# Optimization experiments

Hardware: AMD Instinct MI355X
Metric: run time of the kernel (lower is better)

## Reference

```python
import jax, jax.numpy as jnp
import numpy as np

N_O = 50000
N_Q = 50000
E = 1_600_000
POS_DIM = 3
LATENT = 128
HEADS = 4
HEAD_DIM = 32
EDGE_IN = 3 * POS_DIM  # ['rel','q_pos','o_pos']


def setup_inputs() -> dict:
    key = jax.random.key(0)
    ks = jax.random.split(key, 12)
    h_obs = jax.random.normal(ks[0], (N_O, LATENT), dtype=jnp.float32)
    pos_obs = jax.random.uniform(ks[1], (N_O, POS_DIM), dtype=jnp.float32)
    pos_query = jax.random.uniform(ks[2], (N_Q, POS_DIM), dtype=jnp.float32)
    src = jax.random.randint(ks[3], (E,), 0, N_O, dtype=jnp.int32)
    dst = jnp.sort(jax.random.randint(ks[4], (E,), 0, N_Q, dtype=jnp.int32))
    s = 0.05
    W1 = jax.random.normal(ks[5], (EDGE_IN, LATENT), dtype=jnp.float32) * s
    b1 = jnp.zeros((LATENT,), dtype=jnp.float32)
    W2 = jax.random.normal(ks[6], (LATENT, HEADS), dtype=jnp.float32) * s
    b2 = jnp.zeros((HEADS,), dtype=jnp.float32)
    Wv = jax.random.normal(ks[7], (LATENT, HEADS * HEAD_DIM), dtype=jnp.float32) * s
    bv = jnp.zeros((HEADS * HEAD_DIM,), dtype=jnp.float32)
    log_sigma = jnp.float32(-2.0)
    return {"h_obs": h_obs, "pos_obs": pos_obs, "pos_query": pos_query,
            "src": src, "dst": dst,
            "W1": W1, "b1": b1, "W2": W2, "b2": b2,
            "Wv": Wv, "bv": bv, "log_sigma": log_sigma}


def _forward(h_obs, pos_obs, pos_query, src, dst, W1, b1, W2, b2, Wv, bv, log_sigma):
    pos_o = pos_obs[src]                      # [E, P]
    pos_q = pos_query[dst]                    # [E, P]
    rel = pos_q - pos_o
    edge_attr = jnp.concatenate([rel, pos_q, pos_o], axis=-1)   # [E, 3P]
    hid = jax.nn.relu(edge_attr @ W1 + b1)                      # [E, LATENT]
    logits = hid @ W2 + b2                                      # [E, H]
    dist2 = jnp.sum(rel * rel, axis=-1, keepdims=True)          # [E, 1]
    sigma = jnp.exp(log_sigma) + 1e-6
    logits = logits - dist2 / (2.0 * sigma * sigma)             # kernel log-weight
    # segment softmax over edges grouped by dst
    n_q = pos_query.shape[0]
    m = jax.ops.segment_max(logits, dst, num_segments=n_q)      # [N_q, H]
    ex = jnp.exp(logits - m[dst])
    denom = jax.ops.segment_sum(ex, dst, num_segments=n_q)      # [N_q, H]
    attn = ex / (denom[dst] + 1e-16)                            # [E, H]
    v = (h_obs @ Wv + bv).reshape(-1, HEADS, HEAD_DIM)          # [N_o, H, D]
    msg = attn[:, :, None] * v[src]                             # [E, H, D]
    out = jax.ops.segment_sum(msg, dst, num_segments=n_q)       # [N_q, H, D]
    return out.reshape(n_q, HEADS * HEAD_DIM)


def reference(h_obs, pos_obs, pos_query, src, dst, W1, b1, W2, b2, Wv, bv, log_sigma):
    return _forward(h_obs, pos_obs, pos_query, src, dst, W1, b1, W2, b2, Wv, bv, log_sigma)
```

## Files before the change

kernel.cpp:

```cpp
#include <hip/hip_runtime.h>
#include <hip/hip_bf16.h>
#include <cstdint>
#include <cstddef>

#define N_O 50000
#define N_Q 50000
#define NE  1600000

typedef __attribute__((ext_vector_type(8)))  short short8;
typedef __attribute__((ext_vector_type(16))) float f32x16;

__device__ inline unsigned short f2bf(float x) {
    __hip_bfloat16 hb = __float2bfloat16(x);
    return *reinterpret_cast<unsigned short*>(&hb);
}

__global__ void pack_kernel(const float* __restrict__ W1, const float* __restrict__ b1,
                            const float* __restrict__ W2, const float* __restrict__ b2,
                            const float* __restrict__ log_sigma,
                            unsigned short* __restrict__ W1cT,
                            unsigned short* __restrict__ W2tb,
                            float* __restrict__ scal) {
    int j = threadIdx.x;
    if (j < 128) {
        #pragma unroll
        for (int a = 0; a < 3; ++a) {
            W1cT[j * 8 + a]     = f2bf(W1[(3 + a) * 128 + j] + W1[a * 128 + j]);
            W1cT[j * 8 + 3 + a] = f2bf(W1[(6 + a) * 128 + j] - W1[a * 128 + j]);
        }
        W1cT[j * 8 + 6] = f2bf(b1[j]);
        W1cT[j * 8 + 7] = 0;
        #pragma unroll
        for (int hd = 0; hd < 4; ++hd)
            W2tb[hd * 128 + j] = f2bf(W2[j * 4 + hd]);
    } else if (j == 128) {
        float sigma = expf(log_sigma[0]) + 1e-6f;
        scal[0] = 1.0f / (2.0f * sigma * sigma);
        scal[1] = b2[0]; scal[2] = b2[1]; scal[3] = b2[2]; scal[4] = b2[3];
    }
}

__global__ void rowptr_kernel(const int* __restrict__ dst, int* __restrict__ rp) {
    int q = blockIdx.x * blockDim.x + threadIdx.x;
    if (q > N_Q) return;
    int lo = 0, hi = NE;
    while (lo < hi) {
        int mid = (lo + hi) >> 1;
        if (dst[mid] < q) lo = mid + 1; else hi = mid;
    }
    rp[q] = lo;
}

__global__ __launch_bounds__(256) void vproj_kernel(const float* __restrict__ h,
                                                    const float* __restrict__ Wv,
                                                    const float* __restrict__ bv,
                                                    unsigned short* __restrict__ v) {
    __shared__ float Ash[64 * 132];
    int t = threadIdx.x;
    int n0 = blockIdx.x * 64;
    #pragma unroll
    for (int rep = 0; rep < 8; ++rep) {
        int idx = rep * 256 + t;
        int row = idx >> 5, c4 = (idx & 31) * 4;
        float4 val = make_float4(0.f, 0.f, 0.f, 0.f);
        if (n0 + row < N_O) val = *(const float4*)(h + (size_t)(n0 + row) * 128 + c4);
        float* d = &Ash[row * 132 + c4];
        d[0] = val.x; d[1] = val.y; d[2] = val.z; d[3] = val.w;
    }
    __syncthreads();

    int cg = t & 15, rg = t >> 4;
    int c0 = cg * 8, r0 = rg * 4;
    float acc[4][8];
    #pragma unroll
    for (int i = 0; i < 4; ++i)
        #pragma unroll
        for (int j = 0; j < 8; ++j) acc[i][j] = 0.f;

    const float4* Wv4 = (const float4*)Wv;
    for (int k = 0; k < 128; ++k) {
        float4 b0 = Wv4[k * 32 + cg * 2];
        float4 b1v = Wv4[k * 32 + cg * 2 + 1];
        float bb[8] = {b0.x, b0.y, b0.z, b0.w, b1v.x, b1v.y, b1v.z, b1v.w};
        #pragma unroll
        for (int i = 0; i < 4; ++i) {
            float a = Ash[(r0 + i) * 132 + k];
            #pragma unroll
            for (int j = 0; j < 8; ++j) acc[i][j] += a * bb[j];
        }
    }

    float bvv[8];
    #pragma unroll
    for (int j = 0; j < 8; ++j) bvv[j] = bv[c0 + j];
    #pragma unroll
    for (int i = 0; i < 4; ++i) {
        int n = n0 + r0 + i;
        if (n < N_O) {
            uint4 o;
            __hip_bfloat162 t0 = __float22bfloat162_rn(
                make_float2(acc[i][0] + bvv[0], acc[i][1] + bvv[1]));
            __hip_bfloat162 t1 = __float22bfloat162_rn(
                make_float2(acc[i][2] + bvv[2], acc[i][3] + bvv[3]));
            __hip_bfloat162 t2 = __float22bfloat162_rn(
                make_float2(acc[i][4] + bvv[4], acc[i][5] + bvv[5]));
            __hip_bfloat162 t3 = __float22bfloat162_rn(
                make_float2(acc[i][6] + bvv[6], acc[i][7] + bvv[7]));
            o.x = *reinterpret_cast<unsigned int*>(&t0);
            o.y = *reinterpret_cast<unsigned int*>(&t1);
            o.z = *reinterpret_cast<unsigned int*>(&t2);
            o.w = *reinterpret_cast<unsigned int*>(&t3);
            *(uint4*)(v + (size_t)n * 128 + c0) = o;
        }
    }
}

__global__ __launch_bounds__(256) void edge_kernel(const float* __restrict__ pos_obs,
                                                   const float* __restrict__ pos_query,
                                                   const int* __restrict__ src,
                                                   const int* __restrict__ dst,
                                                   const unsigned short* __restrict__ W1cT,
                                                   const unsigned short* __restrict__ W2tb,
                                                   const float* __restrict__ scal,
                                                   float* __restrict__ logitsT) {
    __shared__ __align__(16) unsigned char smem[4 * 8448];
    int t = threadIdx.x;
    int wave = t >> 6, lane = t & 63;
    int i = lane & 31, h = lane >> 5;
    unsigned char* myrow = smem + wave * 8448 + i * 264;

    short8 zero8;
    #pragma unroll
    for (int k = 0; k < 8; ++k) zero8[k] = 0;

    short8 a1[4];
    #pragma unroll
    for (int b = 0; b < 4; ++b)
        a1[b] = (h == 0) ? *(const short8*)(W1cT + (32 * b + i) * 8) : zero8;

    short8 a2[8];
    #pragma unroll
    for (int m = 0; m < 8; ++m)
        a2[m] = (i < 4) ? *(const short8*)(W2tb + i * 128 + m * 16 + h * 8) : zero8;

    int e = blockIdx.x * 128 + wave * 32 + i;
    int s = src[e], d = dst[e];
    float pox = pos_obs[s * 3 + 0], poy = pos_obs[s * 3 + 1], poz = pos_obs[s * 3 + 2];
    float pqx = pos_query[d * 3 + 0], pqy = pos_query[d * 3 + 1], pqz = pos_query[d * 3 + 2];
    float rx = pqx - pox, ry = pqy - poy, rz = pqz - poz;
    float dist2 = rx * rx + ry * ry + rz * rz;

    short8 bea = zero8;
    if (h == 0) {
        bea[0] = (short)f2bf(pqx); bea[1] = (short)f2bf(pqy); bea[2] = (short)f2bf(pqz);
        bea[3] = (short)f2bf(pox); bea[4] = (short)f2bf(poy); bea[5] = (short)f2bf(poz);
        bea[6] = (short)0x3F80;
        bea[7] = 0;
    }

    f32x16 c1[4];
    #pragma unroll
    for (int b = 0; b < 4; ++b) {
        #pragma unroll
        for (int k = 0; k < 16; ++k) c1[b][k] = 0.0f;
        c1[b] = __builtin_amdgcn_mfma_f32_32x32x16_bf16(a1[b], bea, c1[b], 0, 0, 0);
    }

    #pragma unroll
    for (int b = 0; b < 4; ++b) {
        #pragma unroll
        for (int s_ = 0; s_ < 4; ++s_) {
            float x0 = fmaxf(c1[b][4 * s_ + 0], 0.f);
            float x1 = fmaxf(c1[b][4 * s_ + 1], 0.f);
            float x2 = fmaxf(c1[b][4 * s_ + 2], 0.f);
            float x3 = fmaxf(c1[b][4 * s_ + 3], 0.f);
            __hip_bfloat162 p0 = __float22bfloat162_rn(make_float2(x0, x1));
            __hip_bfloat162 p1 = __float22bfloat162_rn(make_float2(x2, x3));
            uint2 w;
            w.x = *reinterpret_cast<unsigned int*>(&p0);
            w.y = *reinterpret_cast<unsigned int*>(&p1);
            *(uint2*)(myrow + 64 * b + 16 * s_ + 8 * h) = w;
        }
    }

    f32x16 c2;
    #pragma unroll
    for (int k = 0; k < 16; ++k) c2[k] = 0.0f;
    #pragma unroll
    for (int m = 0; m < 8; ++m) {
        uint2 lo = *(const uint2*)(myrow + 32 * m + 16 * h);
        uint2 hi = *(const uint2*)(myrow + 32 * m + 16 * h + 8);
        union { unsigned int u[4]; short8 s; } bf;
        bf.u[0] = lo.x; bf.u[1] = lo.y; bf.u[2] = hi.x; bf.u[3] = hi.y;
        c2 = __builtin_amdgcn_mfma_f32_32x32x16_bf16(a2[m], bf.s, c2, 0, 0, 0);
    }

    if (h == 0) {
        float pen = dist2 * scal[0];
        logitsT[0 * NE + e] = c2[0] + scal[1] - pen;
        logitsT[1 * NE + e] = c2[1] + scal[2] - pen;
        logitsT[2 * NE + e] = c2[2] + scal[3] - pen;
        logitsT[3 * NE + e] = c2[3] + scal[4] - pen;
    }
}

__global__ __launch_bounds__(256) void attn_kernel(const __hip_bfloat162* __restrict__ vb,
                                                   const float* __restrict__ logitsT,
                                                   const int* __restrict__ src,
                                                   const int* __restrict__ rp,
                                                   float* __restrict__ out) {
    int t = threadIdx.x;
    int lane = t & 63;
    int q = blockIdx.x * 4 + (t >> 6);
    int s0 = rp[q], s1 = rp[q + 1];
    int h = lane >> 4, i = lane & 15;
    const float* lp = logitsT + (size_t)h * NE;

    float m = -INFINITY;
    for (int e = s0 + i; e < s1; e += 16) m = fmaxf(m, lp[e]);
    #pragma unroll
    for (int off = 8; off; off >>= 1) m = fmaxf(m, __shfl_xor(m, off));

    float sum = 0.f;
    for (int e = s0 + i; e < s1; e += 16) sum += __expf(lp[e] - m);
    #pragma unroll
    for (int off = 8; off; off >>= 1) sum += __shfl_xor(sum, off);
    float r = 1.0f / (sum + 1e-16f);

    float acc0 = 0.f, acc1 = 0.f;
    int e = s0;
    for (; e < s1 && (e & 3); ++e) {
        float w = __expf(lp[e] - m);
        float2 f = __bfloat1622float2(vb[(size_t)src[e] * 64 + lane]);
        acc0 += w * f.x; acc1 += w * f.y;
    }
    for (; e + 4 <= s1; e += 4) {
        float4 l4 = *(const float4*)(lp + e);
        int4 s4 = *(const int4*)(src + e);
        float w0 = __expf(l4.x - m);
        float w1 = __expf(l4.y - m);
        float w2 = __expf(l4.z - m);
        float w3 = __expf(l4.w - m);
        float2 f0 = __bfloat1622float2(vb[(size_t)s4.x * 64 + lane]);
        float2 f1 = __bfloat1622float2(vb[(size_t)s4.y * 64 + lane]);
        float2 f2 = __bfloat1622float2(vb[(size_t)s4.z * 64 + lane]);
        float2 f3 = __bfloat1622float2(vb[(size_t)s4.w * 64 + lane]);
        acc0 += w0 * f0.x + w1 * f1.x + w2 * f2.x + w3 * f3.x;
        acc1 += w0 * f0.y + w1 * f1.y + w2 * f2.y + w3 * f3.y;
    }
    for (; e < s1; ++e) {
        float w = __expf(lp[e] - m);
        float2 f = __bfloat1622float2(vb[(size_t)src[e] * 64 + lane]);
        acc0 += w * f.x; acc1 += w * f.y;
    }
    *(float2*)(out + (size_t)q * 128 + lane * 2) = make_float2(acc0 * r, acc1 * r);
}

extern "C" void kernel_launch(void* const* d_in, const int* in_sizes, int n_in,
                              void* d_out, int out_size, void* d_ws, size_t ws_size,
                              hipStream_t stream) {
    const float* h_obs     = (const float*)d_in[0];
    const float* pos_obs   = (const float*)d_in[1];
    const float* pos_query = (const float*)d_in[2];
    const int*   src       = (const int*)d_in[3];
    const int*   dst       = (const int*)d_in[4];
    const float* W1        = (const float*)d_in[5];
    const float* b1        = (const float*)d_in[6];
    const float* W2        = (const float*)d_in[7];
    const float* b2        = (const float*)d_in[8];
    const float* Wv        = (const float*)d_in[9];
    const float* bv        = (const float*)d_in[10];
    const float* log_sigma = (const float*)d_in[11];
    float* out = (float*)d_out;

    char* ws = (char*)d_ws;
    int*            rp      = (int*)(ws + 0);
    float*          scal    = (float*)(ws + 200192);
    unsigned short* W1cT    = (unsigned short*)(ws + 200256);
    unsigned short* W2tb    = (unsigned short*)(ws + 202304);
    unsigned short* vbuf    = (unsigned short*)(ws + 208640);
    float*          logitsT = (float*)(ws + 13008768);

    hipLaunchKernelGGL(pack_kernel, dim3(1), dim3(256), 0, stream,
                       W1, b1, W2, b2, log_sigma, W1cT, W2tb, scal);
    hipLaunchKernelGGL(rowptr_kernel, dim3((N_Q + 256) / 256), dim3(256), 0, stream,
                       dst, rp);
    hipLaunchKernelGGL(vproj_kernel, dim3((N_O + 63) / 64), dim3(256), 0, stream,
                       h_obs, Wv, bv, vbuf);
    hipLaunchKernelGGL(edge_kernel, dim3(NE / 128), dim3(256), 0, stream,
                       pos_obs, pos_query, src, dst, W1cT, W2tb, scal, logitsT);
    hipLaunchKernelGGL(attn_kernel, dim3(N_Q / 4), dim3(256), 0, stream,
                       (const __hip_bfloat162*)vbuf, logitsT, src, rp, out);
}
```

Before: 257.4 us.

## Merge edge, vproj and rowptr into one launch; cache softmax weights in LDS

Three independent kernels (edge MLP, value projection, row-pointer search) are folded into one launch that picks a body by block index. This removes two launch boundaries and lets the three jobs run concurrently on the GPU. In the attention kernel, segments with at most 256 edges now store their exp weights in shared memory during the sum pass, so the gather pass reads them back instead of re-reading the logits and recomputing exp. The fused kernel takes the larger shared-memory footprint for every block, and attention now uses extra LDS, which may lower occupancy.

```diff
diff --git a/kernel.cpp b/kernel.cpp
--- a/kernel.cpp
+++ b/kernel.cpp
@@ -6,6 +6,11 @@
 #define N_O 50000
 #define N_Q 50000
 #define NE  1600000
+
+#define EDGE_BLOCKS  (NE / 128)
+#define VP_BLOCKS    ((N_O + 63) / 64)
+#define RP_BLOCKS    ((N_Q + 256) / 256)
+#define WCAP 264
 
 typedef __attribute__((ext_vector_type(8)))  short short8;
 typedef __attribute__((ext_vector_type(16))) float f32x16;
@@ -40,8 +45,8 @@
     }
 }
 
-__global__ void rowptr_kernel(const int* __restrict__ dst, int* __restrict__ rp) {
-    int q = blockIdx.x * blockDim.x + threadIdx.x;
+__device__ void rowptr_body(int bid, const int* __restrict__ dst, int* __restrict__ rp) {
+    int q = bid * 256 + threadIdx.x;
     if (q > N_Q) return;
     int lo = 0, hi = NE;
     while (lo < hi) {
@@ -51,13 +56,13 @@
     rp[q] = lo;
 }
 
-__global__ __launch_bounds__(256) void vproj_kernel(const float* __restrict__ h,
-                                                    const float* __restrict__ Wv,
-                                                    const float* __restrict__ bv,
-                                                    unsigned short* __restrict__ v) {
-    __shared__ float Ash[64 * 132];
+__device__ void vproj_body(int bid, const float* __restrict__ h,
+                           const float* __restrict__ Wv,
+                           const float* __restrict__ bv,
+                           unsigned short* __restrict__ v,
+                           float* Ash ) {
     int t = threadIdx.x;
-    int n0 = blockIdx.x * 64;
+    int n0 = bid * 64;
     #pragma unroll
     for (int rep = 0; rep < 8; ++rep) {
         int idx = rep * 256 + t;
@@ -115,15 +120,15 @@
     }
 }
 
-__global__ __launch_bounds__(256) void edge_kernel(const float* __restrict__ pos_obs,
-                                                   const float* __restrict__ pos_query,
-                                                   const int* __restrict__ src,
-                                                   const int* __restrict__ dst,
-                                                   const unsigned short* __restrict__ W1cT,
-                                                   const unsigned short* __restrict__ W2tb,
-                                                   const float* __restrict__ scal,
-                                                   float* __restrict__ logitsT) {
-    __shared__ __align__(16) unsigned char smem[4 * 8448];
+__device__ void edge_body(int bid, const float* __restrict__ pos_obs,
+                          const float* __restrict__ pos_query,
+                          const int* __restrict__ src,
+                          const int* __restrict__ dst,
+                          const unsigned short* __restrict__ W1cT,
+                          const unsigned short* __restrict__ W2tb,
+                          const float* __restrict__ scal,
+                          float* __restrict__ logitsT,
+                          unsigned char* smem ) {
     int t = threadIdx.x;
     int wave = t >> 6, lane = t & 63;
     int i = lane & 31, h = lane >> 5;
@@ -143,7 +148,7 @@
     for (int m = 0; m < 8; ++m)
         a2[m] = (i < 4) ? *(const short8*)(W2tb + i * 128 + m * 16 + h * 8) : zero8;
 
-    int e = blockIdx.x * 128 + wave * 32 + i;
+    int e = bid * 128 + wave * 32 + i;
     int s = src[e], d = dst[e];
     float pox = pos_obs[s * 3 + 0], poy = pos_obs[s * 3 + 1], poz = pos_obs[s * 3 + 2];
     float pqx = pos_query[d * 3 + 0], pqy = pos_query[d * 3 + 1], pqz = pos_query[d * 3 + 2];
@@ -204,15 +209,41 @@
     }
 }
 
+__global__ __launch_bounds__(256) void fused_kernel(const float* __restrict__ pos_obs,
+                                                    const float* __restrict__ pos_query,
+                                                    const int* __restrict__ src,
+                                                    const int* __restrict__ dst,
+                                                    const unsigned short* __restrict__ W1cT,
+                                                    const unsigned short* __restrict__ W2tb,
+                                                    const float* __restrict__ scal,
+                                                    float* __restrict__ logitsT,
+                                                    const float* __restrict__ h_obs,
+                                                    const float* __restrict__ Wv,
+                                                    const float* __restrict__ bv,
+                                                    unsigned short* __restrict__ vbuf,
+                                                    int* __restrict__ rp) {
+    __shared__ __align__(16) unsigned char smem[33792];
+    int b = blockIdx.x;
+    if (b < EDGE_BLOCKS) {
+        edge_body(b, pos_obs, pos_query, src, dst, W1cT, W2tb, scal, logitsT, smem);
+    } else if (b < EDGE_BLOCKS + VP_BLOCKS) {
+        vproj_body(b - EDGE_BLOCKS, h_obs, Wv, bv, vbuf, (float*)smem);
+    } else {
+        rowptr_body(b - EDGE_BLOCKS - VP_BLOCKS, dst, rp);
+    }
+}
+
 __global__ __launch_bounds__(256) void attn_kernel(const __hip_bfloat162* __restrict__ vb,
                                                    const float* __restrict__ logitsT,
                                                    const int* __restrict__ src,
                                                    const int* __restrict__ rp,
                                                    float* __restrict__ out) {
+    __shared__ __align__(16) float wsh[4 * 4 * WCAP];
     int t = threadIdx.x;
-    int lane = t & 63;
-    int q = blockIdx.x * 4 + (t >> 6);
+    int lane = t & 63, wave = t >> 6;
+    int q = blockIdx.x * 4 + wave;
     int s0 = rp[q], s1 = rp[q + 1];
+    int cnt = s1 - s0;
     int h = lane >> 4, i = lane & 15;
     const float* lp = logitsT + (size_t)h * NE;
 
@@ -221,37 +252,75 @@
     #pragma unroll
     for (int off = 8; off; off >>= 1) m = fmaxf(m, __shfl_xor(m, off));
 
-    float sum = 0.f;
-    for (int e = s0 + i; e < s1; e += 16) sum += __expf(lp[e] - m);
-    #pragma unroll
-    for (int off = 8; off; off >>= 1) sum += __shfl_xor(sum, off);
-    float r = 1.0f / (sum + 1e-16f);
-
-    float acc0 = 0.f, acc1 = 0.f;
-    int e = s0;
-    for (; e < s1 && (e & 3); ++e) {
-        float w = __expf(lp[e] - m);
-        float2 f = __bfloat1622float2(vb[(size_t)src[e] * 64 + lane]);
-        acc0 += w * f.x; acc1 += w * f.y;
-    }
-    for (; e + 4 <= s1; e += 4) {
-        float4 l4 = *(const float4*)(lp + e);
-        int4 s4 = *(const int4*)(src + e);
-        float w0 = __expf(l4.x - m);
-        float w1 = __expf(l4.y - m);
-        float w2 = __expf(l4.z - m);
-        float w3 = __expf(l4.w - m);
-        float2 f0 = __bfloat1622float2(vb[(size_t)s4.x * 64 + lane]);
-        float2 f1 = __bfloat1622float2(vb[(size_t)s4.y * 64 + lane]);
-        float2 f2 = __bfloat1622float2(vb[(size_t)s4.z * 64 + lane]);
-        float2 f3 = __bfloat1622float2(vb[(size_t)s4.w * 64 + lane]);
-        acc0 += w0 * f0.x + w1 * f1.x + w2 * f2.x + w3 * f3.x;
-        acc1 += w0 * f0.y + w1 * f1.y + w2 * f2.y + w3 * f3.y;
-    }
-    for (; e < s1; ++e) {
-        float w = __expf(lp[e] - m);
-        float2 f = __bfloat1622float2(vb[(size_t)src[e] * 64 + lane]);
-        acc0 += w * f.x; acc1 += w * f.y;
+    float acc0 = 0.f, acc1 = 0.f, r;
+
+    if (cnt <= 256) {
+        int s0a = s0 & ~3;
+        float* wpb = wsh + wave * (4 * WCAP) + h * WCAP;
+        float sum = 0.f;
+        for (int e = s0 + i; e < s1; e += 16) {
+            float w = __expf(lp[e] - m);
+            wpb[e - s0a] = w;
+            sum += w;
+        }
+        #pragma unroll
+        for (int off = 8; off; off >>= 1) sum += __shfl_xor(sum, off);
+        r = 1.0f / (sum + 1e-16f);
+
+        int e = s0;
+        int e1 = (s0 + 3) & ~3; if (e1 > s1) e1 = s1;
+        for (; e < e1; ++e) {
+            float w = wpb[e - s0a];
+            float2 f = __bfloat1622float2(vb[(size_t)src[e] * 64 + lane]);
+            acc0 += w * f.x; acc1 += w * f.y;
+        }
+        for (; e + 4 <= s1; e += 4) {
+            float4 w4 = *(const float4*)(wpb + (e - s0a));
+            int4 s4 = *(const int4*)(src + e);
+            float2 f0 = __bfloat1622float2(vb[(size_t)s4.x * 64 + lane]);
+            float2 f1 = __bfloat1622float2(vb[(size_t)s4.y * 64 + lane]);
+            float2 f2 = __bfloat1622float2(vb[(size_t)s4.z * 64 + lane]);
+            float2 f3 = __bfloat1622float2(vb[(size_t)s4.w * 64 + lane]);
+            acc0 += w4.x * f0.x + w4.y * f1.x + w4.z * f2.x + w4.w * f3.x;
+            acc1 += w4.x * f0.y + w4.y * f1.y + w4.z * f2.y + w4.w * f3.y;
+        }
+        for (; e < s1; ++e) {
+            float w = wpb[e - s0a];
+            float2 f = __bfloat1622float2(vb[(size_t)src[e] * 64 + lane]);
+            acc0 += w * f.x; acc1 += w * f.y;
+        }
+    } else {
+        float sum = 0.f;
+        for (int e = s0 + i; e < s1; e += 16) sum += __expf(lp[e] - m);
+        #pragma unroll
+        for (int off = 8; off; off >>= 1) sum += __shfl_xor(sum, off);
+        r = 1.0f / (sum + 1e-16f);
+
+        int e = s0;
+        for (; e < s1 && (e & 3); ++e) {
+            float w = __expf(lp[e] - m);
+            float2 f = __bfloat1622float2(vb[(size_t)src[e] * 64 + lane]);
+            acc0 += w * f.x; acc1 += w * f.y;
+        }
+        for (; e + 4 <= s1; e += 4) {
+            float4 l4 = *(const float4*)(lp + e);
+            int4 s4 = *(const int4*)(src + e);
+            float w0 = __expf(l4.x - m);
+            float w1 = __expf(l4.y - m);
+            float w2 = __expf(l4.z - m);
+            float w3 = __expf(l4.w - m);
+            float2 f0 = __bfloat1622float2(vb[(size_t)s4.x * 64 + lane]);
+            float2 f1 = __bfloat1622float2(vb[(size_t)s4.y * 64 + lane]);
+            float2 f2 = __bfloat1622float2(vb[(size_t)s4.z * 64 + lane]);
+            float2 f3 = __bfloat1622float2(vb[(size_t)s4.w * 64 + lane]);
+            acc0 += w0 * f0.x + w1 * f1.x + w2 * f2.x + w3 * f3.x;
+            acc1 += w0 * f0.y + w1 * f1.y + w2 * f2.y + w3 * f3.y;
+        }
+        for (; e < s1; ++e) {
+            float w = __expf(lp[e] - m);
+            float2 f = __bfloat1622float2(vb[(size_t)src[e] * 64 + lane]);
+            acc0 += w * f.x; acc1 += w * f.y;
+        }
     }
     *(float2*)(out + (size_t)q * 128 + lane * 2) = make_float2(acc0 * r, acc1 * r);
 }
@@ -283,12 +352,10 @@
 
     hipLaunchKernelGGL(pack_kernel, dim3(1), dim3(256), 0, stream,
                        W1, b1, W2, b2, log_sigma, W1cT, W2tb, scal);
-    hipLaunchKernelGGL(rowptr_kernel, dim3((N_Q + 256) / 256), dim3(256), 0, stream,
-                       dst, rp);
-    hipLaunchKernelGGL(vproj_kernel, dim3((N_O + 63) / 64), dim3(256), 0, stream,
-                       h_obs, Wv, bv, vbuf);
-    hipLaunchKernelGGL(edge_kernel, dim3(NE / 128), dim3(256), 0, stream,
-                       pos_obs, pos_query, src, dst, W1cT, W2tb, scal, logitsT);
+    hipLaunchKernelGGL(fused_kernel, dim3(EDGE_BLOCKS + VP_BLOCKS + RP_BLOCKS),
+                       dim3(256), 0, stream,
+                       pos_obs, pos_query, src, dst, W1cT, W2tb, scal, logitsT,
+                       h_obs, Wv, bv, vbuf, rp);
     hipLaunchKernelGGL(attn_kernel, dim3(N_Q / 4), dim3(256), 0, stream,
                        (const __hip_bfloat162*)vbuf, logitsT, src, rp, out);
 }
```

Measured after the change: 249.1 us. 3.2% less time.
